# Kernel optimization log

Hardware: AMD Instinct MI355X
Metric: run time of the kernel (lower is better)

Reference implementation:

```python
import jax, jax.numpy as jnp
import numpy as np

N, E, G = 20000, 400000, 200
IN, HID, OUT, H = 8, 64, 32, 4
EPS = 1e-5
NEG_SLOPE = 0.2


def _gatv2(x, src, dst, Wl, bl, Wr, br, att, bias, n, heads, c):
    # lin_l (source messages) and lin_r (target queries)
    xl = (x @ Wl + bl).reshape(n, heads, c)
    xr = (x @ Wr + br).reshape(n, heads, c)
    # per-edge GATv2 score: att . LeakyReLU(x_l[j] + x_r[i])
    e = jax.nn.leaky_relu(xl[src] + xr[dst], NEG_SLOPE)          # [E,H,C]
    score = jnp.einsum('ehc,hc->eh', e, att)                     # [E,H]
    # softmax over incoming edges of each target node
    m = jax.ops.segment_max(score, dst, num_segments=n)
    ex = jnp.exp(score - m[dst])
    den = jax.ops.segment_sum(ex, dst, num_segments=n)
    alpha = ex / den[dst]                                        # [E,H]
    out = jax.ops.segment_sum(alpha[:, :, None] * xl[src], dst, num_segments=n)
    return out.mean(axis=1) + bias                               # concat=False: head mean


def _layernorm(x, g, b):
    mu = x.mean(-1, keepdims=True)
    var = ((x - mu) ** 2).mean(-1, keepdims=True)
    return (x - mu) * jax.lax.rsqrt(var + EPS) * g + b


def setup_inputs() -> dict:
    key = jax.random.key(0)
    ks = jax.random.split(key, 16)
    s = 0.1
    inp = {
        'x': jax.random.normal(ks[0], (N, IN), jnp.float32),
        'edge_index': jax.random.randint(ks[1], (2, E), 0, N, jnp.int64 if jax.config.jax_enable_x64 else jnp.int32),
        'batch': jnp.sort(jax.random.randint(ks[2], (N,), 0, G)),
        'Wl1': jax.random.normal(ks[3], (IN, H * HID), jnp.float32) * s,
        'bl1': jnp.zeros((H * HID,), jnp.float32),
        'Wr1': jax.random.normal(ks[4], (IN, H * HID), jnp.float32) * s,
        'br1': jnp.zeros((H * HID,), jnp.float32),
        'att1': jax.random.normal(ks[5], (H, HID), jnp.float32) * s,
        'b1': jnp.zeros((HID,), jnp.float32),
        'ln1_g': jnp.ones((HID,), jnp.float32),
        'ln1_b': jnp.zeros((HID,), jnp.float32),
        'Wl2': jax.random.normal(ks[6], (HID, H * OUT), jnp.float32) * s,
        'bl2': jnp.zeros((H * OUT,), jnp.float32),
        'Wr2': jax.random.normal(ks[7], (HID, H * OUT), jnp.float32) * s,
        'br2': jnp.zeros((H * OUT,), jnp.float32),
        'att2': jax.random.normal(ks[8], (H, OUT), jnp.float32) * s,
        'b2': jnp.zeros((OUT,), jnp.float32),
        'ln2_g': jnp.ones((OUT,), jnp.float32),
        'ln2_b': jnp.zeros((OUT,), jnp.float32),
    }
    return inp


def reference(x, edge_index, batch, Wl1, bl1, Wr1, br1, att1, b1, ln1_g, ln1_b,
              Wl2, bl2, Wr2, br2, att2, b2, ln2_g, ln2_b):
    n = x.shape[0]
    loop = jnp.arange(n, dtype=edge_index.dtype)  # add_self_loops=True (PyG default)
    src = jnp.concatenate([edge_index[0], loop])
    dst = jnp.concatenate([edge_index[1], loop])

    h = _gatv2(x, src, dst, Wl1, bl1, Wr1, br1, att1, b1, n, H, HID)
    h = jax.nn.relu(_layernorm(h, ln1_g, ln1_b))
    h = _gatv2(h, src, dst, Wl2, bl2, Wr2, br2, att2, b2, n, H, OUT)
    h = jax.nn.relu(_layernorm(h, ln2_g, ln2_b))

    # global mean pool per graph
    cnt = jax.ops.segment_sum(jnp.ones((n,), h.dtype), batch, num_segments=G)
    pooled = jax.ops.segment_sum(h, batch, num_segments=G)
    return pooled / jnp.maximum(cnt, 1.0)[:, None]
```

## Files before the change

### kernel.cpp

```cpp
#include <hip/hip_runtime.h>
#include <math.h>
#include <stdint.h>

#define NEG_SLOPE 0.2f
#define LN_EPS 1e-5f

typedef __attribute__((ext_vector_type(8))) short short8;
typedef __attribute__((ext_vector_type(4))) float f32x4;

__device__ __forceinline__ uint32_t pack_bf2(float a, float b) {
  uint32_t ua = __float_as_uint(a);
  uint32_t ub = __float_as_uint(b);
  ua = (ua + 0x7fffu + ((ua >> 16) & 1u)) >> 16;
  ub = (ub + 0x7fffu + ((ub >> 16) & 1u)) & 0xffff0000u;
  return ua | ub;
}
__device__ __forceinline__ float2 unpack_bf2(uint32_t u) {
  return make_float2(__uint_as_float(u << 16), __uint_as_float(u & 0xffff0000u));
}
__device__ __forceinline__ uint16_t bf16_rne(float f) {
  uint32_t u = __float_as_uint(f);
  return (uint16_t)((u + 0x7fffu + ((u >> 16) & 1u)) >> 16);
}

__device__ __forceinline__ float row16_sum(float x) {
  x += __int_as_float(__builtin_amdgcn_mov_dpp(__float_as_int(x), 0xB1, 0xF, 0xF, true));
  x += __int_as_float(__builtin_amdgcn_mov_dpp(__float_as_int(x), 0x4E, 0xF, 0xF, true));
  x += __int_as_float(__builtin_amdgcn_mov_dpp(__float_as_int(x), 0x124, 0xF, 0xF, true));
  x += __int_as_float(__builtin_amdgcn_mov_dpp(__float_as_int(x), 0x128, 0xF, 0xF, true));
  return x;
}

__global__ void zero_kernel(int* __restrict__ p, int n) {
  int i = blockIdx.x * blockDim.x + threadIdx.x;
  if (i < n) p[i] = 0;
}

__global__ void hist_kernel(const int* __restrict__ ei, int E, int N, int* __restrict__ cnt) {
  int e = blockIdx.x * blockDim.x + threadIdx.x;
  if (e >= E + N) return;
  int dst = (e < E) ? ei[E + e] : (e - E);
  atomicAdd(&cnt[dst], 1);
}

__global__ __launch_bounds__(1024) void scan_kernel(const int* __restrict__ cnt,
                                                    int* __restrict__ offs,
                                                    int* __restrict__ cursor, int n) {
  __shared__ int wsum[16];
  int tid = threadIdx.x;
  int lane = tid & 63, w = tid >> 6;
  int PER = (n + 1023) >> 10;
  int base = tid * PER;
  int s = 0;
  for (int j = 0; j < PER; ++j) {
    int idx = base + j;
    s += (idx < n) ? cnt[idx] : 0;
  }
  int inc = s;
#pragma unroll
  for (int d = 1; d < 64; d <<= 1) {
    int t = __shfl_up(inc, d, 64);
    if (lane >= d) inc += t;
  }
  if (lane == 63) wsum[w] = inc;
  __syncthreads();
  int wpre = 0;
  for (int j = 0; j < w; ++j) wpre += wsum[j];
  int run = wpre + inc - s;
  for (int j = 0; j < PER; ++j) {
    int idx = base + j;
    if (idx < n) {
      offs[idx] = run;
      cursor[idx] = run;
      run += cnt[idx];
    }
  }
  if (tid == 1023) offs[n] = run;
}

__global__ void scatter_kernel(const int* __restrict__ ei, int E, int N,
                               int* __restrict__ cursor, int* __restrict__ esrc,
                               const float* __restrict__ Wl2, const float* __restrict__ Wr2,
                               uint16_t* __restrict__ Wtb) {
  if (blockIdx.x < 64) {
    int idx = blockIdx.x * 256 + threadIdx.x;
    int c = idx >> 6, k = idx & 63;
    float v = (c < 128) ? Wl2[k * 128 + c] : Wr2[k * 128 + (c - 128)];
    Wtb[idx] = bf16_rne(v);
  }
  int e = blockIdx.x * blockDim.x + threadIdx.x;
  if (e >= E + N) return;
  int src, dst;
  if (e < E) { src = ei[e]; dst = ei[E + e]; }
  else       { src = e - E; dst = src; }
  int pos = atomicAdd(&cursor[dst], 1);
  esrc[pos] = src;
}

__global__ __launch_bounds__(256) void gemm2_mfma_kernel(
    const uint16_t* __restrict__ h1b,
    const uint16_t* __restrict__ Wtb,
    const float* __restrict__ bl, const float* __restrict__ br,
    uint32_t* __restrict__ xl2b, float* __restrict__ xr2, int N) {
  int lane = threadIdx.x & 63;
  int w = threadIdx.x >> 6;
  int c0 = w << 6;
  int l15 = lane & 15, l4 = lane >> 4;
  int node = (blockIdx.x << 4) + l15;
  int nodec = node < N ? node : N - 1;
  const short8* hrow = (const short8*)(h1b + (size_t)nodec * 64);
  short8 b0 = hrow[l4];
  short8 b1 = hrow[4 + l4];
  f32x4 acc[4] = {{0.f,0.f,0.f,0.f},{0.f,0.f,0.f,0.f},{0.f,0.f,0.f,0.f},{0.f,0.f,0.f,0.f}};
#pragma unroll
  for (int t = 0; t < 4; ++t) {
    int row = c0 + (t << 4) + l15;
    const short8* wrow = (const short8*)(Wtb + (size_t)row * 64);
    short8 a0 = wrow[l4];
    short8 a1 = wrow[4 + l4];
    acc[t] = __builtin_amdgcn_mfma_f32_16x16x32_bf16(a0, b0, acc[t], 0, 0, 0);
    acc[t] = __builtin_amdgcn_mfma_f32_16x16x32_bf16(a1, b1, acc[t], 0, 0, 0);
  }
  if (node >= N) return;
  if (c0 < 128) {
#pragma unroll
    for (int t = 0; t < 4; ++t) {
      int q0 = c0 + (t << 4) + (l4 << 2);
      float4 bb = *(const float4*)(bl + q0);
      uint2 pk;
      pk.x = pack_bf2(acc[t][0] + bb.x, acc[t][1] + bb.y);
      pk.y = pack_bf2(acc[t][2] + bb.z, acc[t][3] + bb.w);
      *(uint2*)(xl2b + (size_t)node * 64 + (q0 >> 1)) = pk;
    }
  } else {
#pragma unroll
    for (int t = 0; t < 4; ++t) {
      int q0 = (c0 - 128) + (t << 4) + (l4 << 2);
      float4 bb = *(const float4*)(br + q0);
      float4 v = make_float4(acc[t][0] + bb.x, acc[t][1] + bb.y,
                             acc[t][2] + bb.z, acc[t][3] + bb.w);
      *(float4*)(xr2 + (size_t)node * 128 + q0) = v;
    }
  }
}

__global__ __launch_bounds__(256) void attn1_kernel(
    const float* __restrict__ x,
    const float* __restrict__ Wl, const float* __restrict__ bl,
    const float* __restrict__ Wr, const float* __restrict__ br,
    const float* __restrict__ att, const float* __restrict__ b1,
    const float* __restrict__ g, const float* __restrict__ be,
    const int* __restrict__ offs, const int* __restrict__ esrc,
    uint32_t* __restrict__ h1b, int N) {
  const float L2E = 1.4426950408889634f;
  int lane = threadIdx.x & 63;
  int i = blockIdx.x * (blockDim.x >> 6) + (threadIdx.x >> 6);
  if (i >= N) return;
  int cq = lane & 15;
  const float4* xf4 = (const float4*)x;
  float4 wl[8];
#pragma unroll
  for (int k = 0; k < 8; ++k) wl[k] = ((const float4*)(Wl + k * 256))[lane];
  float4 attq = ((const float4*)att)[lane];
  float4 a4 = make_float4(0.4f * L2E * attq.x, 0.4f * L2E * attq.y,
                          0.4f * L2E * attq.z, 0.4f * L2E * attq.w);
  float4 xa = xf4[(size_t)i * 2], xbv = xf4[(size_t)i * 2 + 1];
  float xs[8] = {xa.x, xa.y, xa.z, xa.w, xbv.x, xbv.y, xbv.z, xbv.w};
  float4 xr = ((const float4*)br)[lane];
#pragma unroll
  for (int k = 0; k < 8; ++k) {
    float4 wr = ((const float4*)(Wr + k * 256))[lane];
    xr.x = fmaf(xs[k], wr.x, xr.x);
    xr.y = fmaf(xs[k], wr.y, xr.y);
    xr.z = fmaf(xs[k], wr.z, xr.z);
    xr.w = fmaf(xs[k], wr.w, xr.w);
  }
  float4 tb = ((const float4*)bl)[lane];
  tb.x += xr.x; tb.y += xr.y; tb.z += xr.z; tb.w += xr.w;

  float dA = 0.f, dB = 0.f;
  float4 accA = make_float4(0.f, 0.f, 0.f, 0.f);
  float4 accB = make_float4(0.f, 0.f, 0.f, 0.f);
  int beg = offs[i], end = offs[i + 1];
  int p = beg;

#define EDGE1(XA, XB, DD, ACC)                                                 \
  {                                                                            \
    float ks0 = XA.x, ks1 = XA.y, ks2 = XA.z, ks3 = XA.w;                      \
    float ks4 = XB.x, ks5 = XB.y, ks6 = XB.z, ks7 = XB.w;                      \
    float kk[8] = {ks0, ks1, ks2, ks3, ks4, ks5, ks6, ks7};                    \
    float4 t = tb;                                                             \
    _Pragma("unroll")                                                          \
    for (int k = 0; k < 8; ++k) {                                              \
      t.x = fmaf(kk[k], wl[k].x, t.x);                                         \
      t.y = fmaf(kk[k], wl[k].y, t.y);                                         \
      t.z = fmaf(kk[k], wl[k].z, t.z);                                         \
      t.w = fmaf(kk[k], wl[k].w, t.w);                                         \
    }                                                                          \
    float u0 = fmaf(1.5f, t.x, fabsf(t.x));                                    \
    float u1 = fmaf(1.5f, t.y, fabsf(t.y));                                    \
    float u2 = fmaf(1.5f, t.z, fabsf(t.z));                                    \
    float u3 = fmaf(1.5f, t.w, fabsf(t.w));                                    \
    float sc = a4.x * u0;                                                      \
    sc = fmaf(a4.y, u1, sc);                                                   \
    sc = fmaf(a4.z, u2, sc);                                                   \
    sc = fmaf(a4.w, u3, sc);                                                   \
    sc = row16_sum(sc);                                                        \
    float wgt = exp2f(sc);                                                     \
    DD += wgt;                                                                 \
    ACC.x = fmaf(wgt, t.x, ACC.x);                                             \
    ACC.y = fmaf(wgt, t.y, ACC.y);                                             \
    ACC.z = fmaf(wgt, t.z, ACC.z);                                             \
    ACC.w = fmaf(wgt, t.w, ACC.w);                                             \
  }

  for (; p + 3 < end; p += 4) {
    int s0 = __builtin_amdgcn_readfirstlane(esrc[p]);
    int s1 = __builtin_amdgcn_readfirstlane(esrc[p + 1]);
    int s2 = __builtin_amdgcn_readfirstlane(esrc[p + 2]);
    int s3 = __builtin_amdgcn_readfirstlane(esrc[p + 3]);
    float4 xa0 = xf4[(size_t)s0 * 2], xb0 = xf4[(size_t)s0 * 2 + 1];
    float4 xa1 = xf4[(size_t)s1 * 2], xb1 = xf4[(size_t)s1 * 2 + 1];
    float4 xa2 = xf4[(size_t)s2 * 2], xb2 = xf4[(size_t)s2 * 2 + 1];
    float4 xa3 = xf4[(size_t)s3 * 2], xb3 = xf4[(size_t)s3 * 2 + 1];
    EDGE1(xa0, xb0, dA, accA)
    EDGE1(xa1, xb1, dB, accB)
    EDGE1(xa2, xb2, dA, accA)
    EDGE1(xa3, xb3, dB, accB)
  }
  for (; p < end; ++p) {
    int s0 = __builtin_amdgcn_readfirstlane(esrc[p]);
    float4 xa0 = xf4[(size_t)s0 * 2], xb0 = xf4[(size_t)s0 * 2 + 1];
    EDGE1(xa0, xb0, dA, accA)
  }
#undef EDGE1

  float inv = 1.0f / (dA + dB);
  float v0 = (accA.x + accB.x) * inv - xr.x;
  float v1 = (accA.y + accB.y) * inv - xr.y;
  float v2 = (accA.z + accB.z) * inv - xr.z;
  float v3 = (accA.w + accB.w) * inv - xr.w;
  v0 += __shfl_xor(v0, 16, 64); v0 += __shfl_xor(v0, 32, 64);
  v1 += __shfl_xor(v1, 16, 64); v1 += __shfl_xor(v1, 32, 64);
  v2 += __shfl_xor(v2, 16, 64); v2 += __shfl_xor(v2, 32, 64);
  v3 += __shfl_xor(v3, 16, 64); v3 += __shfl_xor(v3, 32, 64);
  float4 b1q = ((const float4*)b1)[cq];
  v0 = 0.25f * v0 + b1q.x;
  v1 = 0.25f * v1 + b1q.y;
  v2 = 0.25f * v2 + b1q.z;
  v3 = 0.25f * v3 + b1q.w;
  float s1 = row16_sum(v0 + v1 + v2 + v3);
  float mu = s1 * (1.0f / 64.0f);
  float d0 = v0 - mu, d1 = v1 - mu, d2 = v2 - mu, d3 = v3 - mu;
  float s2 = row16_sum(d0 * d0 + d1 * d1 + d2 * d2 + d3 * d3);
  float rstd = rsqrtf(s2 * (1.0f / 64.0f) + LN_EPS);
  float4 gq = ((const float4*)g)[cq];
  float4 beq = ((const float4*)be)[cq];
  float y0 = fmaxf(fmaf(d0 * rstd, gq.x, beq.x), 0.f);
  float y1 = fmaxf(fmaf(d1 * rstd, gq.y, beq.y), 0.f);
  float y2 = fmaxf(fmaf(d2 * rstd, gq.z, beq.z), 0.f);
  float y3 = fmaxf(fmaf(d3 * rstd, gq.w, beq.w), 0.f);
  if (lane < 16) {
    uint2 pk;
    pk.x = pack_bf2(y0, y1);
    pk.y = pack_bf2(y2, y3);
    *(uint2*)(h1b + (size_t)i * 32 + cq * 2) = pk;
  }
}

__global__ __launch_bounds__(256) void attn2_kernel(
    const uint32_t* __restrict__ xl2b, const float* __restrict__ xr2,
    const float* __restrict__ att, const float* __restrict__ b2,
    const float* __restrict__ g, const float* __restrict__ be,
    const int* __restrict__ offs, const int* __restrict__ esrc,
    const int* __restrict__ batch, float* __restrict__ pooled, int N) {
  const float L2E = 1.4426950408889634f;
  int lane = threadIdx.x & 63;
  int i = blockIdx.x * (blockDim.x >> 6) + (threadIdx.x >> 6);
  if (i >= N) return;
  int cq = lane & 15;
  float2 attq = ((const float2*)att)[lane];
  float2 a4 = make_float2(0.4f * L2E * attq.x, 0.4f * L2E * attq.y);
  float2 xrq = ((const float2*)xr2)[(size_t)i * 64 + lane];
  float dA = 0.f, aA0 = 0.f, aA1 = 0.f;
  float dB = 0.f, aB0 = 0.f, aB1 = 0.f;
  int beg = offs[i], end = offs[i + 1];
  int p = beg;

#define EDGE2(U, DD, A0, A1)                                                   \
  {                                                                            \
    float2 e0 = unpack_bf2(U);                                                 \
    float t0 = e0.x + xrq.x, t1 = e0.y + xrq.y;                                \
    float u0 = fmaf(1.5f, t0, fabsf(t0));                                      \
    float u1 = fmaf(1.5f, t1, fabsf(t1));                                      \
    float sc = fmaf(a4.y, u1, a4.x * u0);                                      \
    sc = row16_sum(sc);                                                        \
    float wgt = exp2f(sc);                                                     \
    DD += wgt;                                                                 \
    A0 = fmaf(wgt, e0.x, A0); A1 = fmaf(wgt, e0.y, A1);                        \
  }

  for (; p + 3 < end; p += 4) {
    int s0 = __builtin_amdgcn_readfirstlane(esrc[p]);
    int s1 = __builtin_amdgcn_readfirstlane(esrc[p + 1]);
    int s2 = __builtin_amdgcn_readfirstlane(esrc[p + 2]);
    int s3 = __builtin_amdgcn_readfirstlane(esrc[p + 3]);
    uint32_t u0 = (xl2b + (size_t)s0 * 64)[lane];
    uint32_t u1 = (xl2b + (size_t)s1 * 64)[lane];
    uint32_t u2 = (xl2b + (size_t)s2 * 64)[lane];
    uint32_t u3 = (xl2b + (size_t)s3 * 64)[lane];
    EDGE2(u0, dA, aA0, aA1)
    EDGE2(u1, dB, aB0, aB1)
    EDGE2(u2, dA, aA0, aA1)
    EDGE2(u3, dB, aB0, aB1)
  }
  for (; p < end; ++p) {
    int s0 = __builtin_amdgcn_readfirstlane(esrc[p]);
    uint32_t u0 = (xl2b + (size_t)s0 * 64)[lane];
    EDGE2(u0, dA, aA0, aA1)
  }
#undef EDGE2

  float inv = 1.0f / (dA + dB);
  float v0 = (aA0 + aB0) * inv;
  float v1 = (aA1 + aB1) * inv;
  v0 += __shfl_xor(v0, 16, 64); v0 += __shfl_xor(v0, 32, 64);
  v1 += __shfl_xor(v1, 16, 64); v1 += __shfl_xor(v1, 32, 64);
  float2 b2q = ((const float2*)b2)[cq];
  v0 = 0.25f * v0 + b2q.x;
  v1 = 0.25f * v1 + b2q.y;
  float s1 = row16_sum(v0 + v1);
  float mu = s1 * (1.0f / 32.0f);
  float d0 = v0 - mu, d1 = v1 - mu;
  float s2 = row16_sum(d0 * d0 + d1 * d1);
  float rstd = rsqrtf(s2 * (1.0f / 32.0f) + LN_EPS);
  float2 gq = ((const float2*)g)[cq];
  float2 beq = ((const float2*)be)[cq];
  float y0 = fmaxf(fmaf(d0 * rstd, gq.x, beq.x), 0.f);
  float y1 = fmaxf(fmaf(d1 * rstd, gq.y, beq.y), 0.f);
  if (lane < 16) {
    int gi = batch[i];
    atomicAdd(&pooled[gi * 32 + 2 * cq], y0);
    atomicAdd(&pooled[gi * 32 + 2 * cq + 1], y1);
  }
}

__global__ void final_kernel(const float* __restrict__ pooled, const int* __restrict__ batch,
                             float* __restrict__ out, int N) {
  int gidx = blockIdx.x;
  int a = 0, b = N;
  while (a < b) { int m = (a + b) >> 1; if (batch[m] < gidx) a = m + 1; else b = m; }
  int lo = a;
  b = N;
  while (a < b) { int m = (a + b) >> 1; if (batch[m] < gidx + 1) a = m + 1; else b = m; }
  int cntv = a - lo;
  float inv = 1.0f / (float)(cntv > 0 ? cntv : 1);
  out[gidx * 32 + threadIdx.x] = pooled[gidx * 32 + threadIdx.x] * inv;
}

extern "C" void kernel_launch(void* const* d_in, const int* in_sizes, int n_in,
                              void* d_out, int out_size, void* d_ws, size_t ws_size,
                              hipStream_t stream) {
  const float* x    = (const float*)d_in[0];
  const int*   ei   = (const int*)d_in[1];
  const int*   batch= (const int*)d_in[2];
  const float* Wl1  = (const float*)d_in[3];
  const float* bl1  = (const float*)d_in[4];
  const float* Wr1  = (const float*)d_in[5];
  const float* br1  = (const float*)d_in[6];
  const float* att1 = (const float*)d_in[7];
  const float* b1   = (const float*)d_in[8];
  const float* ln1g = (const float*)d_in[9];
  const float* ln1b = (const float*)d_in[10];
  const float* Wl2  = (const float*)d_in[11];
  const float* bl2  = (const float*)d_in[12];
  const float* Wr2  = (const float*)d_in[13];
  const float* br2  = (const float*)d_in[14];
  const float* att2 = (const float*)d_in[15];
  const float* b2   = (const float*)d_in[16];
  const float* ln2g = (const float*)d_in[17];
  const float* ln2b = (const float*)d_in[18];

  int N = in_sizes[0] / 8;
  int E = in_sizes[1] / 2;
  int G = out_size / 32;

  char* ws = (char*)d_ws;
  size_t off = 0;
  auto alloc = [&](size_t bytes) -> void* {
    void* p = (void*)(ws + off);
    off += (bytes + 255) & ~(size_t)255;
    return p;
  };
  int*      cnt    = (int*)alloc((size_t)N * 4);
  float*    pooled = (float*)alloc((size_t)G * 32 * 4);
  int*      offs   = (int*)alloc((size_t)(N + 1) * 4);
  int*      cursor = (int*)alloc((size_t)N * 4);
  int*      esrc   = (int*)alloc((size_t)(E + N) * 4);
  uint32_t* h1b    = (uint32_t*)alloc((size_t)N * 64 * 2);
  uint16_t* Wtb    = (uint16_t*)alloc((size_t)256 * 64 * 2);
  uint32_t* xl2b   = (uint32_t*)alloc((size_t)N * 64 * 4);
  float*    xr2    = (float*)alloc((size_t)N * 128 * 4);

  int zero_ints = (int)(((char*)(pooled + (size_t)G * 32) - (char*)cnt) / 4);
  int tot = E + N;
  zero_kernel<<<(zero_ints + 255) / 256, 256, 0, stream>>>(cnt, zero_ints);
  hist_kernel<<<(tot + 255) / 256, 256, 0, stream>>>(ei, E, N, cnt);
  scan_kernel<<<1, 1024, 0, stream>>>(cnt, offs, cursor, N);
  scatter_kernel<<<(tot + 255) / 256, 256, 0, stream>>>(ei, E, N, cursor, esrc,
                                                        Wl2, Wr2, Wtb);

  attn1_kernel<<<(N + 3) / 4, 256, 0, stream>>>(x, Wl1, bl1, Wr1, br1, att1, b1,
                                                ln1g, ln1b, offs, esrc, h1b, N);
  gemm2_mfma_kernel<<<(N + 15) / 16, 256, 0, stream>>>((const uint16_t*)h1b, Wtb, bl2, br2,
                                                       xl2b, xr2, N);
  attn2_kernel<<<(N + 3) / 4, 256, 0, stream>>>(xl2b, xr2, att2, b2, ln2g, ln2b,
                                                offs, esrc, batch, pooled, N);

  final_kernel<<<G, 32, 0, stream>>>(pooled, batch, (float*)d_out, N);
}
```

Baseline: 187.3 us.

## Compute layer-1 edge scores with bf16 MFMA over 16-edge tiles

Rewrites the first attention kernel so each wave handles 16 edges at once. It computes the per-edge xl projection with bf16 MFMA instructions against a padded bf16 copy of Wl1 staged in LDS, instead of per-edge scalar FMAs. The weighted aggregation is done on the raw 8-dim inputs and projected through Wl1 only once at the end, which uses linearity to avoid accumulating 256-wide vectors per edge. A prep pass converts x to padded bf16 and pre-scales att1, and the layer-2 loop drops readfirstlane on the gathered indices. This trades fp32 exactness of the scores for bf16 rounding and adds LDS staging and padded-lane waste when a node has few edges.

```diff
diff --git a/kernel.cpp b/kernel.cpp
--- a/kernel.cpp
+++ b/kernel.cpp
@@ -2,8 +2,8 @@
 #include <math.h>
 #include <stdint.h>
 
-#define NEG_SLOPE 0.2f
 #define LN_EPS 1e-5f
+#define L2E 1.4426950408889634f
 
 typedef __attribute__((ext_vector_type(8))) short short8;
 typedef __attribute__((ext_vector_type(4))) float f32x4;
@@ -36,11 +36,25 @@
   if (i < n) p[i] = 0;
 }
 
-__global__ void hist_kernel(const int* __restrict__ ei, int E, int N, int* __restrict__ cnt) {
-  int e = blockIdx.x * blockDim.x + threadIdx.x;
-  if (e >= E + N) return;
-  int dst = (e < E) ? ei[E + e] : (e - E);
-  atomicAdd(&cnt[dst], 1);
+__global__ void prep_hist_kernel(const int* __restrict__ ei, int E, int N,
+                                 int* __restrict__ cnt,
+                                 const float* __restrict__ x, uint16_t* __restrict__ xb16) {
+  int tid = blockIdx.x * blockDim.x + threadIdx.x;
+  if (tid < N) {
+    const float4* xf4 = (const float4*)x;
+    float4 a = xf4[(size_t)tid * 2], b = xf4[(size_t)tid * 2 + 1];
+    uint32_t* row = (uint32_t*)(xb16 + (size_t)tid * 32);
+    row[0] = pack_bf2(a.x, a.y);
+    row[1] = pack_bf2(a.z, a.w);
+    row[2] = pack_bf2(b.x, b.y);
+    row[3] = pack_bf2(b.z, b.w);
+#pragma unroll
+    for (int j = 4; j < 16; ++j) row[j] = 0;
+  }
+  if (tid < E + N) {
+    int dst = (tid < E) ? ei[E + tid] : (tid - E);
+    atomicAdd(&cnt[dst], 1);
+  }
 }
 
 __global__ __launch_bounds__(1024) void scan_kernel(const int* __restrict__ cnt,
@@ -81,12 +95,20 @@
 __global__ void scatter_kernel(const int* __restrict__ ei, int E, int N,
                                int* __restrict__ cursor, int* __restrict__ esrc,
                                const float* __restrict__ Wl2, const float* __restrict__ Wr2,
-                               uint16_t* __restrict__ Wtb) {
+                               uint16_t* __restrict__ Wtb,
+                               const float* __restrict__ Wl1, uint16_t* __restrict__ Wb1pad,
+                               const float* __restrict__ att1, float* __restrict__ att1s) {
   if (blockIdx.x < 64) {
     int idx = blockIdx.x * 256 + threadIdx.x;
     int c = idx >> 6, k = idx & 63;
     float v = (c < 128) ? Wl2[k * 128 + c] : Wr2[k * 128 + (c - 128)];
     Wtb[idx] = bf16_rne(v);
+  } else if (blockIdx.x < 96) {
+    int idx = (blockIdx.x - 64) * 256 + threadIdx.x;
+    int ch = idx >> 5, k = idx & 31;
+    Wb1pad[idx] = (k < 8) ? bf16_rne(Wl1[k * 256 + ch]) : (uint16_t)0;
+  } else if (blockIdx.x == 96) {
+    if (threadIdx.x < 256) att1s[threadIdx.x] = 0.4f * L2E * att1[threadIdx.x];
   }
   int e = blockIdx.x * blockDim.x + threadIdx.x;
   if (e >= E + N) return;
@@ -144,107 +166,134 @@
   }
 }
 
-__global__ __launch_bounds__(256) void attn1_kernel(
+__global__ __launch_bounds__(256) void attn1_mfma_kernel(
     const float* __restrict__ x,
     const float* __restrict__ Wl, const float* __restrict__ bl,
     const float* __restrict__ Wr, const float* __restrict__ br,
-    const float* __restrict__ att, const float* __restrict__ b1,
+    const uint16_t* __restrict__ xb16, const uint16_t* __restrict__ Wb1pad,
+    const float* __restrict__ att1s, const float* __restrict__ b1,
     const float* __restrict__ g, const float* __restrict__ be,
     const int* __restrict__ offs, const int* __restrict__ esrc,
     uint32_t* __restrict__ h1b, int N) {
-  const float L2E = 1.4426950408889634f;
+  __shared__ float4   ltb[4 * 64];
+  __shared__ uint16_t lW[256 * 40];
   int lane = threadIdx.x & 63;
-  int i = blockIdx.x * (blockDim.x >> 6) + (threadIdx.x >> 6);
+  int wid = threadIdx.x >> 6;
+  int l15 = lane & 15, l4 = lane >> 4;
+
+  {
+    int row = threadIdx.x;
+    const uint2* src = (const uint2*)(Wb1pad + (size_t)row * 32);
+    uint2* dst = (uint2*)(lW + (size_t)row * 40);
+#pragma unroll
+    for (int j = 0; j < 8; ++j) dst[j] = src[j];
+  }
+  __syncthreads();
+
+  int i = blockIdx.x * 4 + wid;
   if (i >= N) return;
-  int cq = lane & 15;
   const float4* xf4 = (const float4*)x;
-  float4 wl[8];
-#pragma unroll
-  for (int k = 0; k < 8; ++k) wl[k] = ((const float4*)(Wl + k * 256))[lane];
-  float4 attq = ((const float4*)att)[lane];
-  float4 a4 = make_float4(0.4f * L2E * attq.x, 0.4f * L2E * attq.y,
-                          0.4f * L2E * attq.z, 0.4f * L2E * attq.w);
-  float4 xa = xf4[(size_t)i * 2], xbv = xf4[(size_t)i * 2 + 1];
-  float xs[8] = {xa.x, xa.y, xa.z, xa.w, xbv.x, xbv.y, xbv.z, xbv.w};
+
+  float4 xa_ = xf4[(size_t)i * 2], xb_ = xf4[(size_t)i * 2 + 1];
+  float xs0 = xa_.x, xs1 = xa_.y, xs2 = xa_.z, xs3 = xa_.w;
+  float xs4 = xb_.x, xs5 = xb_.y, xs6 = xb_.z, xs7 = xb_.w;
   float4 xr = ((const float4*)br)[lane];
+  {
+    float xsv[8] = {xs0, xs1, xs2, xs3, xs4, xs5, xs6, xs7};
+#pragma unroll
+    for (int k = 0; k < 8; ++k) {
+      float4 wr = ((const float4*)(Wr + k * 256))[lane];
+      xr.x = fmaf(xsv[k], wr.x, xr.x);
+      xr.y = fmaf(xsv[k], wr.y, xr.y);
+      xr.z = fmaf(xsv[k], wr.z, xr.z);
+      xr.w = fmaf(xsv[k], wr.w, xr.w);
+    }
+  }
+  float4 bl4 = ((const float4*)bl)[lane];
+  float4 tb4 = make_float4(bl4.x + xr.x, bl4.y + xr.y, bl4.z + xr.z, bl4.w + xr.w);
+  ltb[wid * 64 + lane] = tb4;
+  float4 tbm[16];
+#pragma unroll
+  for (int m = 0; m < 16; ++m) tbm[m] = ltb[wid * 64 + 4 * m + l4];
+
+  float den[4] = {0.f, 0.f, 0.f, 0.f};
+  float2 xg[4] = {{0.f, 0.f}, {0.f, 0.f}, {0.f, 0.f}, {0.f, 0.f}};
+
+  int beg = offs[i], end = offs[i + 1];
+  int T = (end - beg + 15) >> 4;
+  for (int tt = 0; tt < T; ++tt) {
+    int eidx = beg + (tt << 4) + l15;
+    bool valid = eidx < end;
+    int ecl = valid ? eidx : end - 1;
+    int s = esrc[ecl];
+    short8 bf = *(const short8*)(xb16 + (size_t)s * 32 + (l4 << 3));
+    float4 xf0 = xf4[(size_t)s * 2], xf1 = xf4[(size_t)s * 2 + 1];
+    float2 xp = (l4 & 2) ? ((l4 & 1) ? make_float2(xf1.z, xf1.w) : make_float2(xf1.x, xf1.y))
+                         : ((l4 & 1) ? make_float2(xf0.z, xf0.w) : make_float2(xf0.x, xf0.y));
+#pragma unroll
+    for (int h = 0; h < 4; ++h) {
+      float sp = 0.f;
+#pragma unroll
+      for (int mm = 0; mm < 4; ++mm) {
+        int m = 4 * h + mm;
+        short8 af = *(const short8*)(lW + (size_t)(16 * m + l15) * 40 + (l4 << 3));
+        f32x4 zz = {0.f, 0.f, 0.f, 0.f};
+        f32x4 ac = __builtin_amdgcn_mfma_f32_16x16x32_bf16(af, bf, zz, 0, 0, 0);
+        float4 tv = tbm[m];
+        float t0 = ac[0] + tv.x, t1 = ac[1] + tv.y, t2 = ac[2] + tv.z, t3 = ac[3] + tv.w;
+        float u0 = fmaf(1.5f, t0, fabsf(t0));
+        float u1 = fmaf(1.5f, t1, fabsf(t1));
+        float u2 = fmaf(1.5f, t2, fabsf(t2));
+        float u3 = fmaf(1.5f, t3, fabsf(t3));
+        float4 av = *(const float4*)(att1s + (m << 4) + (l4 << 2));
+        sp = fmaf(av.x, u0, sp);
+        sp = fmaf(av.y, u1, sp);
+        sp = fmaf(av.z, u2, sp);
+        sp = fmaf(av.w, u3, sp);
+      }
+      sp += __shfl_xor(sp, 16, 64);
+      sp += __shfl_xor(sp, 32, 64);
+      float w = valid ? exp2f(sp) : 0.f;
+      den[h] += w;
+      xg[h].x = fmaf(w, xp.x, xg[h].x);
+      xg[h].y = fmaf(w, xp.y, xg[h].y);
+    }
+  }
+
+#pragma unroll
+  for (int h = 0; h < 4; ++h) {
+    den[h] = row16_sum(den[h]);
+    xg[h].x = row16_sum(xg[h].x);
+    xg[h].y = row16_sum(xg[h].y);
+  }
+
+  float4 v4 = make_float4(0.f, 0.f, 0.f, 0.f);
 #pragma unroll
   for (int k = 0; k < 8; ++k) {
-    float4 wr = ((const float4*)(Wr + k * 256))[lane];
-    xr.x = fmaf(xs[k], wr.x, xr.x);
-    xr.y = fmaf(xs[k], wr.y, xr.y);
-    xr.z = fmaf(xs[k], wr.z, xr.z);
-    xr.w = fmaf(xs[k], wr.w, xr.w);
-  }
-  float4 tb = ((const float4*)bl)[lane];
-  tb.x += xr.x; tb.y += xr.y; tb.z += xr.z; tb.w += xr.w;
-
-  float dA = 0.f, dB = 0.f;
-  float4 accA = make_float4(0.f, 0.f, 0.f, 0.f);
-  float4 accB = make_float4(0.f, 0.f, 0.f, 0.f);
-  int beg = offs[i], end = offs[i + 1];
-  int p = beg;
-
-#define EDGE1(XA, XB, DD, ACC)                                                 \
-  {                                                                            \
-    float ks0 = XA.x, ks1 = XA.y, ks2 = XA.z, ks3 = XA.w;                      \
-    float ks4 = XB.x, ks5 = XB.y, ks6 = XB.z, ks7 = XB.w;                      \
-    float kk[8] = {ks0, ks1, ks2, ks3, ks4, ks5, ks6, ks7};                    \
-    float4 t = tb;                                                             \
-    _Pragma("unroll")                                                          \
-    for (int k = 0; k < 8; ++k) {                                              \
-      t.x = fmaf(kk[k], wl[k].x, t.x);                                         \
-      t.y = fmaf(kk[k], wl[k].y, t.y);                                         \
-      t.z = fmaf(kk[k], wl[k].z, t.z);                                         \
-      t.w = fmaf(kk[k], wl[k].w, t.w);                                         \
-    }                                                                          \
-    float u0 = fmaf(1.5f, t.x, fabsf(t.x));                                    \
-    float u1 = fmaf(1.5f, t.y, fabsf(t.y));                                    \
-    float u2 = fmaf(1.5f, t.z, fabsf(t.z));                                    \
-    float u3 = fmaf(1.5f, t.w, fabsf(t.w));                                    \
-    float sc = a4.x * u0;                                                      \
-    sc = fmaf(a4.y, u1, sc);                                                   \
-    sc = fmaf(a4.z, u2, sc);                                                   \
-    sc = fmaf(a4.w, u3, sc);                                                   \
-    sc = row16_sum(sc);                                                        \
-    float wgt = exp2f(sc);                                                     \
-    DD += wgt;                                                                 \
-    ACC.x = fmaf(wgt, t.x, ACC.x);                                             \
-    ACC.y = fmaf(wgt, t.y, ACC.y);                                             \
-    ACC.z = fmaf(wgt, t.z, ACC.z);                                             \
-    ACC.w = fmaf(wgt, t.w, ACC.w);                                             \
-  }
-
-  for (; p + 3 < end; p += 4) {
-    int s0 = __builtin_amdgcn_readfirstlane(esrc[p]);
-    int s1 = __builtin_amdgcn_readfirstlane(esrc[p + 1]);
-    int s2 = __builtin_amdgcn_readfirstlane(esrc[p + 2]);
-    int s3 = __builtin_amdgcn_readfirstlane(esrc[p + 3]);
-    float4 xa0 = xf4[(size_t)s0 * 2], xb0 = xf4[(size_t)s0 * 2 + 1];
-    float4 xa1 = xf4[(size_t)s1 * 2], xb1 = xf4[(size_t)s1 * 2 + 1];
-    float4 xa2 = xf4[(size_t)s2 * 2], xb2 = xf4[(size_t)s2 * 2 + 1];
-    float4 xa3 = xf4[(size_t)s3 * 2], xb3 = xf4[(size_t)s3 * 2 + 1];
-    EDGE1(xa0, xb0, dA, accA)
-    EDGE1(xa1, xb1, dB, accB)
-    EDGE1(xa2, xb2, dA, accA)
-    EDGE1(xa3, xb3, dB, accB)
-  }
-  for (; p < end; ++p) {
-    int s0 = __builtin_amdgcn_readfirstlane(esrc[p]);
-    float4 xa0 = xf4[(size_t)s0 * 2], xb0 = xf4[(size_t)s0 * 2 + 1];
-    EDGE1(xa0, xb0, dA, accA)
-  }
-#undef EDGE1
-
-  float inv = 1.0f / (dA + dB);
-  float v0 = (accA.x + accB.x) * inv - xr.x;
-  float v1 = (accA.y + accB.y) * inv - xr.y;
-  float v2 = (accA.z + accB.z) * inv - xr.z;
-  float v3 = (accA.w + accB.w) * inv - xr.w;
+    int srcl = (k >> 1) << 4;
+    float c0 = __shfl((k & 1) ? xg[0].y : xg[0].x, srcl, 64);
+    float c1 = __shfl((k & 1) ? xg[1].y : xg[1].x, srcl, 64);
+    float c2 = __shfl((k & 1) ? xg[2].y : xg[2].x, srcl, 64);
+    float c3 = __shfl((k & 1) ? xg[3].y : xg[3].x, srcl, 64);
+    float xsel = (l4 & 2) ? ((l4 & 1) ? c3 : c2) : ((l4 & 1) ? c1 : c0);
+    float4 wlv = ((const float4*)(Wl + k * 256))[lane];
+    v4.x = fmaf(wlv.x, xsel, v4.x);
+    v4.y = fmaf(wlv.y, xsel, v4.y);
+    v4.z = fmaf(wlv.z, xsel, v4.z);
+    v4.w = fmaf(wlv.w, xsel, v4.w);
+  }
+  float dsel = (l4 & 2) ? ((l4 & 1) ? den[3] : den[2]) : ((l4 & 1) ? den[1] : den[0]);
+  float inv = 1.0f / dsel;
+  float v0 = fmaf(v4.x, inv, bl4.x);
+  float v1 = fmaf(v4.y, inv, bl4.y);
+  float v2 = fmaf(v4.z, inv, bl4.z);
+  float v3 = fmaf(v4.w, inv, bl4.w);
+
   v0 += __shfl_xor(v0, 16, 64); v0 += __shfl_xor(v0, 32, 64);
   v1 += __shfl_xor(v1, 16, 64); v1 += __shfl_xor(v1, 32, 64);
   v2 += __shfl_xor(v2, 16, 64); v2 += __shfl_xor(v2, 32, 64);
   v3 += __shfl_xor(v3, 16, 64); v3 += __shfl_xor(v3, 32, 64);
-  float4 b1q = ((const float4*)b1)[cq];
+  float4 b1q = ((const float4*)b1)[l15];
   v0 = 0.25f * v0 + b1q.x;
   v1 = 0.25f * v1 + b1q.y;
   v2 = 0.25f * v2 + b1q.z;
@@ -254,8 +303,8 @@
   float d0 = v0 - mu, d1 = v1 - mu, d2 = v2 - mu, d3 = v3 - mu;
   float s2 = row16_sum(d0 * d0 + d1 * d1 + d2 * d2 + d3 * d3);
   float rstd = rsqrtf(s2 * (1.0f / 64.0f) + LN_EPS);
-  float4 gq = ((const float4*)g)[cq];
-  float4 beq = ((const float4*)be)[cq];
+  float4 gq = ((const float4*)g)[l15];
+  float4 beq = ((const float4*)be)[l15];
   float y0 = fmaxf(fmaf(d0 * rstd, gq.x, beq.x), 0.f);
   float y1 = fmaxf(fmaf(d1 * rstd, gq.y, beq.y), 0.f);
   float y2 = fmaxf(fmaf(d2 * rstd, gq.z, beq.z), 0.f);
@@ -264,7 +313,7 @@
     uint2 pk;
     pk.x = pack_bf2(y0, y1);
     pk.y = pack_bf2(y2, y3);
-    *(uint2*)(h1b + (size_t)i * 32 + cq * 2) = pk;
+    *(uint2*)(h1b + (size_t)i * 32 + l15 * 2) = pk;
   }
 }
 
@@ -274,7 +323,6 @@
     const float* __restrict__ g, const float* __restrict__ be,
     const int* __restrict__ offs, const int* __restrict__ esrc,
     const int* __restrict__ batch, float* __restrict__ pooled, int N) {
-  const float L2E = 1.4426950408889634f;
   int lane = threadIdx.x & 63;
   int i = blockIdx.x * (blockDim.x >> 6) + (threadIdx.x >> 6);
   if (i >= N) return;
@@ -301,22 +349,19 @@
   }
 
   for (; p + 3 < end; p += 4) {
-    int s0 = __builtin_amdgcn_readfirstlane(esrc[p]);
-    int s1 = __builtin_amdgcn_readfirstlane(esrc[p + 1]);
-    int s2 = __builtin_amdgcn_readfirstlane(esrc[p + 2]);
-    int s3 = __builtin_amdgcn_readfirstlane(esrc[p + 3]);
-    uint32_t u0 = (xl2b + (size_t)s0 * 64)[lane];
-    uint32_t u1 = (xl2b + (size_t)s1 * 64)[lane];
-    uint32_t u2 = (xl2b + (size_t)s2 * 64)[lane];
-    uint32_t u3 = (xl2b + (size_t)s3 * 64)[lane];
+    int s0 = esrc[p], s1 = esrc[p + 1], s2 = esrc[p + 2], s3 = esrc[p + 3];
+    uint32_t u0 = xl2b[(uint32_t)s0 * 64u + lane];
+    uint32_t u1 = xl2b[(uint32_t)s1 * 64u + lane];
+    uint32_t u2 = xl2b[(uint32_t)s2 * 64u + lane];
+    uint32_t u3 = xl2b[(uint32_t)s3 * 64u + lane];
     EDGE2(u0, dA, aA0, aA1)
     EDGE2(u1, dB, aB0, aB1)
     EDGE2(u2, dA, aA0, aA1)
     EDGE2(u3, dB, aB0, aB1)
   }
   for (; p < end; ++p) {
-    int s0 = __builtin_amdgcn_readfirstlane(esrc[p]);
-    uint32_t u0 = (xl2b + (size_t)s0 * 64)[lane];
+    int s0 = esrc[p];
+    uint32_t u0 = xl2b[(uint32_t)s0 * 64u + lane];
     EDGE2(u0, dA, aA0, aA1)
   }
 #undef EDGE2
@@ -397,6 +442,9 @@
   int*      offs   = (int*)alloc((size_t)(N + 1) * 4);
   int*      cursor = (int*)alloc((size_t)N * 4);
   int*      esrc   = (int*)alloc((size_t)(E + N) * 4);
+  uint16_t* xb16   = (uint16_t*)alloc((size_t)N * 32 * 2);
+  uint16_t* Wb1pad = (uint16_t*)alloc((size_t)256 * 32 * 2);
+  float*    att1s  = (float*)alloc((size_t)256 * 4);
   uint32_t* h1b    = (uint32_t*)alloc((size_t)N * 64 * 2);
   uint16_t* Wtb    = (uint16_t*)alloc((size_t)256 * 64 * 2);
   uint32_t* xl2b   = (uint32_t*)alloc((size_t)N * 64 * 4);
@@ -405,13 +453,15 @@
   int zero_ints = (int)(((char*)(pooled + (size_t)G * 32) - (char*)cnt) / 4);
   int tot = E + N;
   zero_kernel<<<(zero_ints + 255) / 256, 256, 0, stream>>>(cnt, zero_ints);
-  hist_kernel<<<(tot + 255) / 256, 256, 0, stream>>>(ei, E, N, cnt);
+  prep_hist_kernel<<<(tot + 255) / 256, 256, 0, stream>>>(ei, E, N, cnt, x, xb16);
   scan_kernel<<<1, 1024, 0, stream>>>(cnt, offs, cursor, N);
   scatter_kernel<<<(tot + 255) / 256, 256, 0, stream>>>(ei, E, N, cursor, esrc,
-                                                        Wl2, Wr2, Wtb);
-
-  attn1_kernel<<<(N + 3) / 4, 256, 0, stream>>>(x, Wl1, bl1, Wr1, br1, att1, b1,
-                                                ln1g, ln1b, offs, esrc, h1b, N);
+                                                        Wl2, Wr2, Wtb, Wl1, Wb1pad,
+                                                        att1, att1s);
+
+  attn1_mfma_kernel<<<(N + 3) / 4, 256, 0, stream>>>(x, Wl1, bl1, Wr1, br1,
+                                                     xb16, Wb1pad, att1s, b1,
+                                                     ln1g, ln1b, offs, esrc, h1b, N);
   gemm2_mfma_kernel<<<(N + 15) / 16, 256, 0, stream>>>((const uint16_t*)h1b, Wtb, bl2, br2,
                                                        xl2b, xr2, N);
   attn2_kernel<<<(N + 3) / 4, 256, 0, stream>>>(xl2b, xr2, att2, b2, ln2g, ln2b,
```

Result: slower. 202.7 us (+8.2%).
